# Kernel tuning notes

Hardware: AMD Instinct MI355X
Metric: run time of the kernel (lower is better)

Reference implementation:

```python
import jax, jax.numpy as jnp
import numpy as np

H, W = 256, 256
S, S_IDX, END_BIAS = 48, 3, 10
E_IDX = S - END_BIAS          # 38
N_ITER = E_IDX - (S_IDX + 1)  # 34 sequential segments after the start segment
OUT_WIN = 10                  # outlier1d window length
OUT_THRESH = 2.0


def setup_inputs() -> dict:
    key = jax.random.key(0)
    # (x, y) event coordinates in [0, W) x [0, H); t/p/b columns are unused by the module.
    events = jax.random.uniform(key, (16, 960000, 2), jnp.float32, minval=0.0, maxval=256.0)
    return {"events": events}


def _blur(a):
    """5x5 uniform (0.04) blur, SAME padding; a: [B, S, D] -> [B, S, D]."""
    k = jnp.full((1, 1, 5, 5), 0.04, jnp.float32)
    return jax.lax.conv_general_dilated(a[:, None], k, (1, 1), [(2, 2), (2, 2)])[:, 0]


def _outlier_flags(m):
    """outlier1d(m[b, si:si+10], thresh=2)[0] for si in [S_IDX+1, E_IDX). m: [B,S] -> bool [B,N_ITER]."""
    widx = (jnp.arange(N_ITER)[:, None] + S_IDX + 1) + jnp.arange(OUT_WIN)[None, :]
    w = m[:, widx]                                   # [B, N_ITER, 10]
    med = jnp.median(w, axis=-1, keepdims=True)
    diff = jnp.abs(w - med)
    mad = jnp.median(diff, axis=-1)                  # [B, N_ITER]
    return 0.6745 * diff[..., 0] / mad > OUT_THRESH


def reference(events):
    B, N, _ = events.shape
    segmentLen = N // S            # static python int
    Nu = segmentLen * S
    x = events[:, :Nu, 0].astype(jnp.int32)   # [B, Nu]
    y = events[:, :Nu, 1].astype(jnp.int32)
    chunks = jnp.repeat(jnp.arange(S), segmentLen)   # segment id per event, [Nu]
    bidx = jnp.arange(B)[:, None]

    # per-batch x-t / y-t histograms via scatter-add
    alongX = jnp.zeros((B, S, W), jnp.float32).at[bidx, chunks[None, :], x].add(1.0)
    alongY = jnp.zeros((B, S, H), jnp.float32).at[bidx, chunks[None, :], y].add(1.0)

    def proc_axis(along, D):
        flat = along.reshape(B, -1)
        cv = (flat.mean(-1) + 3.0 * jnp.std(flat, axis=-1, ddof=1))[:, None, None]
        a = _blur(jnp.clip(along, 0.0, cv))
        m = jnp.einsum('bsd,d->bs', a, jnp.arange(D, dtype=jnp.float32)) / segmentLen
        start = m[:, S_IDX:S_IDX + 1]
        aligned = jnp.round(m - start - (D // 2 - start)).astype(jnp.int32)
        return m, aligned

    meanX, alignedX = proc_axis(alongX, W)
    meanY, alignedY = proc_axis(alongY, H)
    is_out = _outlier_flags(meanX) | _outlier_flags(meanY)   # [B, N_ITER]

    def per_batch(xb, yb, aX, aY, outb):
        xs = jnp.clip(xb - aX[chunks], 0, W - 1)
        ys = jnp.clip(yb - aY[chunks], 0, H - 1)
        idx_c = (xs + W * ys).reshape(S, segmentLen)
        idx_v = (xs // 2 + (W // 2) * (ys // 2)).reshape(S, segmentLen)
        container0 = jnp.zeros(W * H, jnp.int32).at[idx_c[S_IDX]].add(1)
        ver0 = jnp.zeros((W // 2) * (H // 2), bool).at[idx_v[S_IDX]].set(True)

        def step(carry, inp):
            container, ver, stopped = carry
            ic, iv, is_o = inp
            ver_new = ver.at[iv].set(True)
            cnt = jnp.sum(ver_new).astype(jnp.float32)
            new_info = jnp.sum(jnp.logical_xor(ver_new, ver)).astype(jnp.float32)
            brk = new_info / cnt < 0.1
            do = (~stopped) & (~is_o) & (~brk)
            stopped = stopped | ((~stopped) & (~is_o) & brk)
            container = jnp.where(do, container.at[ic].add(1), container)
            ver = jnp.where(do, ver_new, ver)
            return (container, ver, stopped), None

        (container, _, _), _ = jax.lax.scan(
            step, (container0, ver0, jnp.array(False)),
            (idx_c[S_IDX + 1:E_IDX], idx_v[S_IDX + 1:E_IDX], outb))
        c = container.astype(jnp.float32)
        cv = c.mean() + 3.0 * jnp.std(c, ddof=1)
        return jnp.clip(c, 0.0, cv) / cv

    containers = jax.vmap(per_batch)(x, y, alignedX, alignedY, is_out)  # [B, W*H]
    return containers.reshape(B, 1, H, W)
```

## Files before the change

### kernel.cpp

```cpp
#include <hip/hip_runtime.h>

#define NB 16
#define NEV 960000
#define NS 48
#define SEG 20000
#define S_IDX 3
#define E_IDX 38
#define N_ITER 34
#define ND 256
#define NCH 35

__global__ __launch_bounds__(256) void hist_kernel(const float* __restrict__ events,
                                                   float* __restrict__ alongX,
                                                   float* __restrict__ alongY,
                                                   unsigned* __restrict__ compact,
                                                   unsigned* __restrict__ container) {
    __shared__ unsigned hx[ND], hy[ND];
    int tid = threadIdx.x;
    int blk = blockIdx.x;
    int b = blk / NS, c = blk % NS;
    hx[tid] = 0; hy[tid] = 0;
    {
        uint4 z = {0u, 0u, 0u, 0u};
        for (int i = blk * 256 + tid; i < 262144; i += NB * NS * 256)
            ((uint4*)container)[i] = z;
    }
    __syncthreads();
    size_t base = (size_t)b * NEV + (size_t)c * SEG;
    const float4* ev4 = (const float4*)(events + base * 2);
    bool wr = (c >= S_IDX && c < E_IDX);
    unsigned* dst = wr ? compact + ((size_t)b * NCH + (c - S_IDX)) * (SEG / 2) : nullptr;
    for (int k = tid; k < SEG / 2; k += 256) {
        float4 v = ev4[k];
        int x0 = (int)v.x, y0 = (int)v.y, x1 = (int)v.z, y1 = (int)v.w;
        x0 = x0 > 255 ? 255 : x0; y0 = y0 > 255 ? 255 : y0;
        x1 = x1 > 255 ? 255 : x1; y1 = y1 > 255 ? 255 : y1;
        atomicAdd(&hx[x0], 1u); atomicAdd(&hy[y0], 1u);
        atomicAdd(&hx[x1], 1u); atomicAdd(&hy[y1], 1u);
        if (wr) dst[k] = (unsigned)(x0 | (y0 << 8)) | ((unsigned)(x1 | (y1 << 8)) << 16);
    }
    __syncthreads();
    int o = (b * NS + c) * ND + tid;
    alongX[o] = (float)hx[tid];
    alongY[o] = (float)hy[tid];
}

__global__ __launch_bounds__(256) void stats_kernel(const float* __restrict__ alongX,
                                                    const float* __restrict__ alongY,
                                                    int* __restrict__ alignedX,
                                                    int* __restrict__ alignedY,
                                                    float* __restrict__ m_all) {
    __shared__ float sbuf[NS * ND];
    __shared__ double sredA[4], sredB[4];
    __shared__ float scv;
    int tid = threadIdx.x;
    int b = blockIdx.x >> 1, axis = blockIdx.x & 1;
    const float* along = (axis ? alongY : alongX) + (size_t)b * NS * ND;
    for (int k = 0; k < NS; k++) sbuf[k * ND + tid] = along[k * ND + tid];
    __syncthreads();
    double s = 0.0, s2 = 0.0;
    for (int k = 0; k < NS; k++) { double v = sbuf[k * ND + tid]; s += v; s2 += v * v; }
    for (int off = 32; off; off >>= 1) { s += __shfl_down(s, off); s2 += __shfl_down(s2, off); }
    if ((tid & 63) == 0) { sredA[tid >> 6] = s; sredB[tid >> 6] = s2; }
    __syncthreads();
    if (tid == 0) {
        double ts = sredA[0] + sredA[1] + sredA[2] + sredA[3];
        double ts2 = sredB[0] + sredB[1] + sredB[2] + sredB[3];
        const double N = (double)(NS * ND);
        double mean = ts / N;
        double var  = (ts2 - ts * ts / N) / (N - 1.0);
        scv = (float)(mean + 3.0 * sqrt(var));
    }
    __syncthreads();
    float cv = scv;
    int wave = tid >> 6, lane = tid & 63;
    for (int q = 0; q < 12; ++q) {
        int sI = wave * 12 + q;
        double acc = 0.0;
        #pragma unroll
        for (int k = 0; k < 4; ++k) {
            int d = lane + 64 * k;
            int lo = d - 2 < 0 ? 0 : d - 2;
            int hi = d + 2 > 255 ? 255 : d + 2;
            double Wd = 0.5 * (double)(lo + hi) * (double)(hi - lo + 1);
            double t = 0.0;
            #pragma unroll
            for (int ds = -2; ds <= 2; ++ds) {
                int ss = sI + ds;
                if (ss >= 0 && ss < NS) t += (double)fminf(sbuf[ss * ND + d], cv);
            }
            acc += t * Wd;
        }
        for (int off = 32; off; off >>= 1) acc += __shfl_down(acc, off);
        if (lane == 0) {
            float mf = (float)(acc * 0.04 / (double)SEG);
            m_all[(b * 2 + axis) * NS + sI] = mf;
            (axis ? alignedY : alignedX)[b * NS + sI] = (int)rintf(mf - 128.0f);
        }
    }
}

__global__ __launch_bounds__(256) void mask_kernel(const unsigned* __restrict__ compact,
                                                   const int* __restrict__ alignedX,
                                                   const int* __restrict__ alignedY,
                                                   unsigned* __restrict__ masks) {
    __shared__ unsigned sm[512];
    int tid = threadIdx.x, blk = blockIdx.x;
    int b = blk / NCH, ci = blk % NCH, si = S_IDX + ci;
    sm[tid] = 0; sm[tid + 256] = 0;
    __syncthreads();
    int aX = alignedX[b * NS + si], aY = alignedY[b * NS + si];
    const uint4* cp = (const uint4*)(compact + ((size_t)b * NCH + ci) * (SEG / 2));
    for (int i = tid; i < SEG / 8; i += 256) {
        uint4 w = cp[i];
        unsigned ws[4] = {w.x, w.y, w.z, w.w};
        #pragma unroll
        for (int j = 0; j < 4; j++) {
            unsigned v = ws[j];
            #pragma unroll
            for (int h = 0; h < 2; h++) {
                unsigned e = (h ? (v >> 16) : v) & 0xFFFFu;
                int xs = (int)(e & 255u) - aX; xs = xs < 0 ? 0 : (xs > 255 ? 255 : xs);
                int ys = (int)(e >> 8)   - aY; ys = ys < 0 ? 0 : (ys > 255 ? 255 : ys);
                int iv = (xs >> 1) | ((ys >> 1) << 7);
                atomicOr(&sm[iv >> 5], 1u << (iv & 31));
            }
        }
    }
    __syncthreads();
    unsigned* mo = masks + (size_t)blk * 512;
    mo[tid] = sm[tid];
    mo[tid + 256] = sm[tid + 256];
}

__device__ inline float median10(const float* v) {
    float w[10];
    #pragma unroll
    for (int i = 0; i < 10; i++) w[i] = v[i];
    #pragma unroll
    for (int i = 1; i < 10; i++) {
        float k = w[i]; int j = i - 1;
        while (j >= 0 && w[j] > k) { w[j + 1] = w[j]; j--; }
        w[j + 1] = k;
    }
    return 0.5f * (w[4] + w[5]);
}

__device__ inline bool outlier_flag(const float* w) {
    float med = median10(w);
    float d[10];
    #pragma unroll
    for (int i = 0; i < 10; i++) d[i] = fabsf(w[i] - med);
    float d0 = d[0];
    float mad = median10(d);
    return (0.6745f * d0 / mad) > 2.0f;
}

__device__ inline unsigned wave_sum_u32(unsigned v) {
    for (int off = 32; off; off >>= 1) v += __shfl_xor(v, off);
    return v;
}

__global__ __launch_bounds__(64) void decide_kernel(const unsigned* __restrict__ masks,
                                                    const float* __restrict__ m_all,
                                                    unsigned long long* __restrict__ commitmask) {
    int b = blockIdx.x, lane = threadIdx.x;
    bool f = false;
    if (lane < N_ITER) {
        const float* mx = m_all + b * 2 * NS;
        const float* my = mx + NS;
        f = outlier_flag(&mx[S_IDX + 1 + lane]) || outlier_flag(&my[S_IDX + 1 + lane]);
    }
    unsigned long long omask = __ballot(f);
    const unsigned* mb = masks + (size_t)b * NCH * 512;
    uint4 v0 = ((const uint4*)mb)[lane * 2];
    uint4 v1 = ((const uint4*)mb)[lane * 2 + 1];
    unsigned ver[8] = {v0.x, v0.y, v0.z, v0.w, v1.x, v1.y, v1.z, v1.w};
    unsigned pc = 0;
    #pragma unroll
    for (int j = 0; j < 8; j++) pc += __popc(ver[j]);
    unsigned cnt = wave_sum_u32(pc);
    unsigned long long cm = 1ull;
    for (int si = S_IDX + 1; si < E_IDX; ++si) {
        int idx = si - S_IDX;
        const uint4* dp = (const uint4*)(mb + (size_t)idx * 512);
        uint4 d0 = dp[lane * 2], d1 = dp[lane * 2 + 1];
        unsigned del[8] = {d0.x, d0.y, d0.z, d0.w, d1.x, d1.y, d1.z, d1.w};
        unsigned nl = 0;
        #pragma unroll
        for (int j = 0; j < 8; j++) nl += __popc(del[j] & ~ver[j]);
        unsigned ni = wave_sum_u32(nl);
        bool is_o = (omask >> (si - S_IDX - 1)) & 1;
        if (!is_o) {
            unsigned cn = cnt + ni;
            float ratio = (float)ni / (float)cn;
            if (ratio < 0.1f) break;
            cm |= 1ull << idx;
            cnt = cn;
            #pragma unroll
            for (int j = 0; j < 8; j++) ver[j] |= del[j];
        }
    }
    if (lane == 0) commitmask[b] = cm;
}

__global__ __launch_bounds__(256) void commit_kernel(const unsigned* __restrict__ compact,
                                                     const unsigned long long* __restrict__ commitmask,
                                                     unsigned* __restrict__ container) {
    int blk = blockIdx.x, tid = threadIdx.x;
    int b = blk / NCH, ci = blk % NCH;
    if (!((commitmask[b] >> ci) & 1ull)) return;
    int si = S_IDX + ci;
    (void)si;
}

__global__ __launch_bounds__(256) void commit2_kernel(const unsigned* __restrict__ compact,
                                                      const int* __restrict__ alignedX,
                                                      const int* __restrict__ alignedY,
                                                      const unsigned long long* __restrict__ commitmask,
                                                      unsigned* __restrict__ container) {
    int blk = blockIdx.x, tid = threadIdx.x;
    int b = blk / NCH, ci = blk % NCH;
    if (!((commitmask[b] >> ci) & 1ull)) return;
    int si = S_IDX + ci;
    int aX = alignedX[b * NS + si], aY = alignedY[b * NS + si];
    unsigned* cont = container + (size_t)b * 65536;
    const uint4* cp = (const uint4*)(compact + ((size_t)b * NCH + ci) * (SEG / 2));
    for (int i = tid; i < SEG / 8; i += 256) {
        uint4 w = cp[i];
        unsigned ws[4] = {w.x, w.y, w.z, w.w};
        #pragma unroll
        for (int j = 0; j < 4; j++) {
            unsigned v = ws[j];
            #pragma unroll
            for (int h = 0; h < 2; h++) {
                unsigned e = (h ? (v >> 16) : v) & 0xFFFFu;
                int xs = (int)(e & 255u) - aX; xs = xs < 0 ? 0 : (xs > 255 ? 255 : xs);
                int ys = (int)(e >> 8)   - aY; ys = ys < 0 ? 0 : (ys > 255 ? 255 : ys);
                atomicAdd(&cont[xs | (ys << 8)], 1u);
            }
        }
    }
}

__global__ __launch_bounds__(256) void cv_kernel(const unsigned* __restrict__ container,
                                                 float* __restrict__ cvb) {
    __shared__ double sredA[4], sredB[4];
    int tid = threadIdx.x, b = blockIdx.x;
    const uint4* c4 = (const uint4*)(container + (size_t)b * 65536);
    double s = 0.0, s2 = 0.0;
    for (int i = tid; i < 16384; i += 256) {
        uint4 v = c4[i];
        double a0 = v.x, a1 = v.y, a2 = v.z, a3 = v.w;
        s += a0 + a1 + a2 + a3;
        s2 += a0 * a0 + a1 * a1 + a2 * a2 + a3 * a3;
    }
    for (int off = 32; off; off >>= 1) { s += __shfl_down(s, off); s2 += __shfl_down(s2, off); }
    if ((tid & 63) == 0) { sredA[tid >> 6] = s; sredB[tid >> 6] = s2; }
    __syncthreads();
    if (tid == 0) {
        double ts = sredA[0] + sredA[1] + sredA[2] + sredA[3];
        double ts2 = sredB[0] + sredB[1] + sredB[2] + sredB[3];
        double mean = ts / 65536.0;
        double var = (ts2 - ts * ts / 65536.0) / 65535.0;
        cvb[b] = (float)(mean + 3.0 * sqrt(var));
    }
}

__global__ __launch_bounds__(256) void finish_kernel(const unsigned* __restrict__ container,
                                                     const float* __restrict__ cvb,
                                                     float* __restrict__ out) {
    int g = blockIdx.x * 256 + threadIdx.x;
    int b = g >> 14;
    float cv = cvb[b];
    uint4 v = ((const uint4*)container)[g];
    float4 o;
    o.x = fminf((float)v.x, cv) / cv;
    o.y = fminf((float)v.y, cv) / cv;
    o.z = fminf((float)v.z, cv) / cv;
    o.w = fminf((float)v.w, cv) / cv;
    ((float4*)out)[g] = o;
}

extern "C" void kernel_launch(void* const* d_in, const int* in_sizes, int n_in,
                              void* d_out, int out_size, void* d_ws, size_t ws_size,
                              hipStream_t stream) {
    const float* events = (const float*)d_in[0];
    float* out = (float*)d_out;
    char* ws = (char*)d_ws;

    float*    alongX    = (float*)(ws);
    float*    alongY    = (float*)(ws + 786432);
    unsigned* container = (unsigned*)(ws + 1572864);
    int*      alignedX  = (int*)(ws + 5767168);
    int*      alignedY  = (int*)(ws + 5770240);
    float*    m_all     = (float*)(ws + 5773312);
    unsigned long long* commitmask = (unsigned long long*)(ws + 5779456);
    float*    cvb       = (float*)(ws + 5779584);
    unsigned* compact   = (unsigned*)(ws + 6291456);
    unsigned* masks     = (unsigned*)(ws + 29360128);

    hist_kernel<<<NB * NS, 256, 0, stream>>>(events, alongX, alongY, compact, container);
    stats_kernel<<<NB * 2, 256, 0, stream>>>(alongX, alongY, alignedX, alignedY, m_all);
    mask_kernel<<<NB * NCH, 256, 0, stream>>>(compact, alignedX, alignedY, masks);
    decide_kernel<<<NB, 64, 0, stream>>>(masks, m_all, commitmask);
    commit2_kernel<<<NB * NCH, 256, 0, stream>>>(compact, alignedX, alignedY, commitmask, container);
    cv_kernel<<<NB, 256, 0, stream>>>(container, cvb);
    finish_kernel<<<1024, 256, 0, stream>>>(container, cvb, out);
}
```

Before: 295.9 us.

## Split cv reduction across blocks with integer atomics and prefetch masks in decide

```diff
diff --git a/kernel.cpp b/kernel.cpp
--- a/kernel.cpp
+++ b/kernel.cpp
@@ -14,7 +14,8 @@
                                                    float* __restrict__ alongX,
                                                    float* __restrict__ alongY,
                                                    unsigned* __restrict__ compact,
-                                                   unsigned* __restrict__ container) {
+                                                   unsigned* __restrict__ container,
+                                                   unsigned long long* __restrict__ sums) {
     __shared__ unsigned hx[ND], hy[ND];
     int tid = threadIdx.x;
     int blk = blockIdx.x;
@@ -24,6 +25,7 @@
         uint4 z = {0u, 0u, 0u, 0u};
         for (int i = blk * 256 + tid; i < 262144; i += NB * NS * 256)
             ((uint4*)container)[i] = z;
+        if (blk == 0 && tid < NB * 2) sums[tid] = 0ull;
     }
     __syncthreads();
     size_t base = (size_t)b * NEV + (size_t)c * SEG;
@@ -165,6 +167,11 @@
                                                     const float* __restrict__ m_all,
                                                     unsigned long long* __restrict__ commitmask) {
     int b = blockIdx.x, lane = threadIdx.x;
+    const unsigned* mb = masks + (size_t)b * NCH * 512;
+    uint4 v0 = ((const uint4*)mb)[lane * 2];
+    uint4 v1 = ((const uint4*)mb)[lane * 2 + 1];
+    const uint4* pp = (const uint4*)(mb + 512);
+    uint4 p0 = pp[lane * 2], p1 = pp[lane * 2 + 1];
     bool f = false;
     if (lane < N_ITER) {
         const float* mx = m_all + b * 2 * NS;
@@ -172,25 +179,24 @@
         f = outlier_flag(&mx[S_IDX + 1 + lane]) || outlier_flag(&my[S_IDX + 1 + lane]);
     }
     unsigned long long omask = __ballot(f);
-    const unsigned* mb = masks + (size_t)b * NCH * 512;
-    uint4 v0 = ((const uint4*)mb)[lane * 2];
-    uint4 v1 = ((const uint4*)mb)[lane * 2 + 1];
     unsigned ver[8] = {v0.x, v0.y, v0.z, v0.w, v1.x, v1.y, v1.z, v1.w};
     unsigned pc = 0;
     #pragma unroll
     for (int j = 0; j < 8; j++) pc += __popc(ver[j]);
     unsigned cnt = wave_sum_u32(pc);
     unsigned long long cm = 1ull;
-    for (int si = S_IDX + 1; si < E_IDX; ++si) {
-        int idx = si - S_IDX;
-        const uint4* dp = (const uint4*)(mb + (size_t)idx * 512);
-        uint4 d0 = dp[lane * 2], d1 = dp[lane * 2 + 1];
-        unsigned del[8] = {d0.x, d0.y, d0.z, d0.w, d1.x, d1.y, d1.z, d1.w};
+    for (int idx = 1; idx < NCH; ++idx) {
+        uint4 c0 = p0, c1 = p1;
+        if (idx + 1 < NCH) {
+            const uint4* np = (const uint4*)(mb + (size_t)(idx + 1) * 512);
+            p0 = np[lane * 2]; p1 = np[lane * 2 + 1];
+        }
+        unsigned del[8] = {c0.x, c0.y, c0.z, c0.w, c1.x, c1.y, c1.z, c1.w};
         unsigned nl = 0;
         #pragma unroll
         for (int j = 0; j < 8; j++) nl += __popc(del[j] & ~ver[j]);
         unsigned ni = wave_sum_u32(nl);
-        bool is_o = (omask >> (si - S_IDX - 1)) & 1;
+        bool is_o = (omask >> (idx - 1)) & 1;
         if (!is_o) {
             unsigned cn = cnt + ni;
             float ratio = (float)ni / (float)cn;
@@ -205,20 +211,10 @@
 }
 
 __global__ __launch_bounds__(256) void commit_kernel(const unsigned* __restrict__ compact,
+                                                     const int* __restrict__ alignedX,
+                                                     const int* __restrict__ alignedY,
                                                      const unsigned long long* __restrict__ commitmask,
                                                      unsigned* __restrict__ container) {
-    int blk = blockIdx.x, tid = threadIdx.x;
-    int b = blk / NCH, ci = blk % NCH;
-    if (!((commitmask[b] >> ci) & 1ull)) return;
-    int si = S_IDX + ci;
-    (void)si;
-}
-
-__global__ __launch_bounds__(256) void commit2_kernel(const unsigned* __restrict__ compact,
-                                                      const int* __restrict__ alignedX,
-                                                      const int* __restrict__ alignedY,
-                                                      const unsigned long long* __restrict__ commitmask,
-                                                      unsigned* __restrict__ container) {
     int blk = blockIdx.x, tid = threadIdx.x;
     int b = blk / NCH, ci = blk % NCH;
     if (!((commitmask[b] >> ci) & 1ull)) return;
@@ -244,35 +240,37 @@
 }
 
 __global__ __launch_bounds__(256) void cv_kernel(const unsigned* __restrict__ container,
-                                                 float* __restrict__ cvb) {
-    __shared__ double sredA[4], sredB[4];
-    int tid = threadIdx.x, b = blockIdx.x;
-    const uint4* c4 = (const uint4*)(container + (size_t)b * 65536);
-    double s = 0.0, s2 = 0.0;
-    for (int i = tid; i < 16384; i += 256) {
+                                                 unsigned long long* __restrict__ sums) {
+    __shared__ unsigned long long sredA[4], sredB[4];
+    int tid = threadIdx.x, blk = blockIdx.x;
+    int b = blk >> 4, part = blk & 15;
+    const uint4* c4 = (const uint4*)(container + (size_t)b * 65536) + part * 1024;
+    unsigned long long s = 0, s2 = 0;
+    for (int i = tid; i < 1024; i += 256) {
         uint4 v = c4[i];
-        double a0 = v.x, a1 = v.y, a2 = v.z, a3 = v.w;
-        s += a0 + a1 + a2 + a3;
-        s2 += a0 * a0 + a1 * a1 + a2 * a2 + a3 * a3;
+        s  += (unsigned long long)v.x + v.y + v.z + v.w;
+        s2 += (unsigned long long)v.x * v.x + (unsigned long long)v.y * v.y
+            + (unsigned long long)v.z * v.z + (unsigned long long)v.w * v.w;
     }
     for (int off = 32; off; off >>= 1) { s += __shfl_down(s, off); s2 += __shfl_down(s2, off); }
     if ((tid & 63) == 0) { sredA[tid >> 6] = s; sredB[tid >> 6] = s2; }
     __syncthreads();
     if (tid == 0) {
-        double ts = sredA[0] + sredA[1] + sredA[2] + sredA[3];
-        double ts2 = sredB[0] + sredB[1] + sredB[2] + sredB[3];
-        double mean = ts / 65536.0;
-        double var = (ts2 - ts * ts / 65536.0) / 65535.0;
-        cvb[b] = (float)(mean + 3.0 * sqrt(var));
+        atomicAdd(&sums[b * 2],     sredA[0] + sredA[1] + sredA[2] + sredA[3]);
+        atomicAdd(&sums[b * 2 + 1], sredB[0] + sredB[1] + sredB[2] + sredB[3]);
     }
 }
 
 __global__ __launch_bounds__(256) void finish_kernel(const unsigned* __restrict__ container,
-                                                     const float* __restrict__ cvb,
+                                                     const unsigned long long* __restrict__ sums,
                                                      float* __restrict__ out) {
     int g = blockIdx.x * 256 + threadIdx.x;
     int b = g >> 14;
-    float cv = cvb[b];
+    double ts  = (double)sums[b * 2];
+    double ts2 = (double)sums[b * 2 + 1];
+    double mean = ts / 65536.0;
+    double var  = (ts2 - ts * ts / 65536.0) / 65535.0;
+    float cv = (float)(mean + 3.0 * sqrt(var));
     uint4 v = ((const uint4*)container)[g];
     float4 o;
     o.x = fminf((float)v.x, cv) / cv;
@@ -296,15 +294,15 @@
     int*      alignedY  = (int*)(ws + 5770240);
     float*    m_all     = (float*)(ws + 5773312);
     unsigned long long* commitmask = (unsigned long long*)(ws + 5779456);
-    float*    cvb       = (float*)(ws + 5779584);
+    unsigned long long* sums       = (unsigned long long*)(ws + 5779584);
     unsigned* compact   = (unsigned*)(ws + 6291456);
     unsigned* masks     = (unsigned*)(ws + 29360128);
 
-    hist_kernel<<<NB * NS, 256, 0, stream>>>(events, alongX, alongY, compact, container);
+    hist_kernel<<<NB * NS, 256, 0, stream>>>(events, alongX, alongY, compact, container, sums);
     stats_kernel<<<NB * 2, 256, 0, stream>>>(alongX, alongY, alignedX, alignedY, m_all);
     mask_kernel<<<NB * NCH, 256, 0, stream>>>(compact, alignedX, alignedY, masks);
     decide_kernel<<<NB, 64, 0, stream>>>(masks, m_all, commitmask);
-    commit2_kernel<<<NB * NCH, 256, 0, stream>>>(compact, alignedX, alignedY, commitmask, container);
-    cv_kernel<<<NB, 256, 0, stream>>>(container, cvb);
-    finish_kernel<<<1024, 256, 0, stream>>>(container, cvb, out);
-}
+    commit_kernel<<<NB * NCH, 256, 0, stream>>>(compact, alignedX, alignedY, commitmask, container);
+    cv_kernel<<<NB * 16, 256, 0, stream>>>(container, sums);
+    finish_kernel<<<1024, 256, 0, stream>>>(container, sums, out);
+}
```

Result: faster. 280.8 us (-5.1%).
